# Kernel optimization log

Measured on AMD Instinct MI355X. Metric: run time of the kernel, lower is better.

Reference implementation:

```python
import jax, jax.numpy as jnp
import numpy as np

B, T, C = 4, 2048, 1024
H = 16
D = C // H  # 64


def setup_inputs() -> dict:
    key = jax.random.key(0)
    k1, k2, k3 = jax.random.split(key, 3)
    x = jax.random.normal(k1, (B, T, C), dtype=jnp.float32)
    W_attn = jax.random.normal(k2, (C, 3 * C), dtype=jnp.float32) * (1.0 / np.sqrt(C))
    W_proj = jax.random.normal(k3, (C, C), dtype=jnp.float32) * (1.0 / np.sqrt(C))
    return {"x": x, "W_attn": W_attn, "W_proj": W_proj}


def reference(x, W_attn, W_proj):
    b, t, c = x.shape
    # qkv projection: [B,T,3C]
    qkv = jnp.einsum('btc,cd->btd', x, W_attn)
    q, k, v = jnp.split(qkv, 3, axis=-1)
    # split heads -> [B,H,T,D]
    q = q.reshape(b, t, H, D).transpose(0, 2, 1, 3)
    k = k.reshape(b, t, H, D).transpose(0, 2, 1, 3)
    v = v.reshape(b, t, H, D).transpose(0, 2, 1, 3)
    # scores scaled by 1/sqrt(C) (faithful to source: uses full embed dim)
    att = jnp.einsum('bhtd,bhsd->bhts', q, k) * (1.0 / jnp.sqrt(jnp.float32(c)))
    # causal mask: -inf where key index > query index
    causal = jnp.tril(jnp.ones((t, t), dtype=bool))
    att = jnp.where(causal, att, jnp.float32(-jnp.inf))
    att = jax.nn.softmax(att, axis=-1)
    # attention output -> combine heads
    y = jnp.einsum('bhts,bhsd->bhtd', att, v)
    y = y.transpose(0, 2, 1, 3).reshape(b, t, c)
    z = jnp.einsum('btc,cd->btd', y, W_proj)
    return z
```

## Files before the change

kernel.cpp:

```cpp
#include <hip/hip_runtime.h>
#include <hip/hip_bf16.h>

typedef __bf16 bf16x8 __attribute__((ext_vector_type(8)));
typedef float f32x4 __attribute__((ext_vector_type(4)));

static __device__ __forceinline__ __bf16 tobf(float x) {
    __hip_bfloat16 h = __float2bfloat16(x);
    __bf16 r;
    __builtin_memcpy(&r, &h, 2);
    return r;
}

static __device__ __forceinline__ float fexp2(float x) {
    float r;
    asm("v_exp_f32 %0, %1" : "=v"(r) : "v"(x));
    return r;
}

__global__ __launch_bounds__(256) void prep_k(const float* __restrict__ x,
                                              __hip_bfloat16* __restrict__ x_bf,
                                              const float* __restrict__ Wa,
                                              __hip_bfloat16* __restrict__ WaT,
                                              const float* __restrict__ Wp,
                                              __hip_bfloat16* __restrict__ WpT) {
    __shared__ float tile[32][33];
    const int bid = blockIdx.x;
    const int tid = threadIdx.x;
    if (bid < 8192) {
        int i = bid * 256 + tid;
        float4 v = reinterpret_cast<const float4*>(x)[i];
        __hip_bfloat16 a = __float2bfloat16(v.x);
        __hip_bfloat16 b = __float2bfloat16(v.y);
        __hip_bfloat16 c = __float2bfloat16(v.z);
        __hip_bfloat16 d = __float2bfloat16(v.w);
        ushort4 o;
        o.x = *reinterpret_cast<unsigned short*>(&a);
        o.y = *reinterpret_cast<unsigned short*>(&b);
        o.z = *reinterpret_cast<unsigned short*>(&c);
        o.w = *reinterpret_cast<unsigned short*>(&d);
        reinterpret_cast<ushort4*>(x_bf)[i] = o;
        return;
    }
    const float* in;
    __hip_bfloat16* out;
    int bx, Cn, qrows;
    float qscale;
    int t;
    if (bid < 8192 + 3072) {
        t = bid - 8192;
        in = Wa; out = WaT; Cn = 3072; qrows = 1024;
        qscale = 0.045084223f;
        bx = t % 96;
    } else {
        t = bid - 11264;
        in = Wp; out = WpT; Cn = 1024; qrows = 0;
        qscale = 1.0f;
        bx = t % 32;
    }
    const int by = (bid < 11264) ? (t / 96) : (t / 32);
    const int R = 1024;
    const int c0 = bx * 32, r0 = by * 32;
    const int tx = tid & 31, ty = tid >> 5;
#pragma unroll
    for (int i = 0; i < 4; ++i)
        tile[ty + i * 8][tx] = in[(size_t)(r0 + ty + i * 8) * Cn + c0 + tx];
    __syncthreads();
#pragma unroll
    for (int i = 0; i < 4; ++i) {
        int orow = c0 + ty + i * 8;
        float v = tile[tx][ty + i * 8];
        if (orow < qrows) v *= qscale;
        out[(size_t)orow * R + r0 + tx] = __float2bfloat16(v);
    }
}

template <bool OUT_BF16, bool FUSE_VT>
__global__ __launch_bounds__(256, 2) void gemm4w(const __hip_bfloat16* __restrict__ A,
                                                 const __hip_bfloat16* __restrict__ Bt,
                                                 __hip_bfloat16* __restrict__ Cb,
                                                 float* __restrict__ Cf,
                                                 __hip_bfloat16* __restrict__ VtOut,
                                                 int M, int N, int K) {
    __shared__ __attribute__((aligned(16))) char As[2][128 * 128];
    __shared__ __attribute__((aligned(16))) char Bs[2][128 * 128];
    const int tid = threadIdx.x;
    const int lane = tid & 63, wid = tid >> 6;
    const int l15 = lane & 15, lg = lane >> 4;
    const int wr = wid >> 1, wc = wid & 1;
    const int lin = blockIdx.y * gridDim.x + blockIdx.x;
    const int cpx = (gridDim.x * gridDim.y) >> 3;
    const int sw = (lin & 7) * cpx + (lin >> 3);
    const int bn = sw % gridDim.x, bm = sw / gridDim.x;
    const size_t arow0 = (size_t)bm * 128;
    const size_t brow0 = (size_t)bn * 128;

    f32x4 acc[4][4] = {};

    const __hip_bfloat16* pa[4];
    const __hip_bfloat16* pb[4];
#pragma unroll
    for (int p = 0; p < 4; ++p) {
        int idx = p * 256 + tid;
        int row = idx >> 3, c = idx & 7;
        int col = 8 * (c ^ (row & 7));
        pa[p] = A + (arow0 + row) * (size_t)K + col;
        pb[p] = Bt + (brow0 + row) * (size_t)K + col;
    }

    auto stage = [&](int buf) {
        char* Ad = buf ? &As[1][0] : &As[0][0];
        char* Bd = buf ? &Bs[1][0] : &Bs[0][0];
#pragma unroll
        for (int p = 0; p < 4; ++p) {
            __builtin_amdgcn_global_load_lds(
                (const __attribute__((address_space(1))) void*)pa[p],
                (__attribute__((address_space(3))) void*)(Ad + (p * 256 + tid) * 16), 16, 0, 0);
            __builtin_amdgcn_global_load_lds(
                (const __attribute__((address_space(1))) void*)pb[p],
                (__attribute__((address_space(3))) void*)(Bd + (p * 256 + tid) * 16), 16, 0, 0);
            pa[p] += 64;
            pb[p] += 64;
        }
    };

    stage(0);
    asm volatile("s_waitcnt vmcnt(0)" ::: "memory");
    __syncthreads();

    const int nk = K >> 6;
    int cur = 0;
    for (int kt = 0; kt < nk; ++kt) {
        if (kt + 1 < nk) stage(cur ^ 1);
        const char* Ab = cur ? &As[1][0] : &As[0][0];
        const char* Bb = cur ? &Bs[1][0] : &Bs[0][0];
#pragma unroll
        for (int ks = 0; ks < 2; ++ks) {
            bf16x8 af[4], bfr[4];
#pragma unroll
            for (int mf = 0; mf < 4; ++mf) {
                int R = wr * 64 + mf * 16 + l15;
                af[mf] = *reinterpret_cast<const bf16x8*>(
                    Ab + R * 128 + 16 * ((ks * 4 + lg) ^ (R & 7)));
            }
#pragma unroll
            for (int nf = 0; nf < 4; ++nf) {
                int R = wc * 64 + nf * 16 + l15;
                bfr[nf] = *reinterpret_cast<const bf16x8*>(
                    Bb + R * 128 + 16 * ((ks * 4 + lg) ^ (R & 7)));
            }
            __builtin_amdgcn_s_setprio(1);
#pragma unroll
            for (int mf = 0; mf < 4; ++mf)
#pragma unroll
                for (int nf = 0; nf < 4; ++nf)
                    acc[mf][nf] = __builtin_amdgcn_mfma_f32_16x16x32_bf16(af[mf], bfr[nf],
                                                                          acc[mf][nf], 0, 0, 0);
            __builtin_amdgcn_s_setprio(0);
        }
        asm volatile("s_waitcnt vmcnt(0)" ::: "memory");
        __syncthreads();
        cur ^= 1;
    }

    if (FUSE_VT && bn >= 16) {
        const int trow0 = bm * 128;
        const int b = trow0 >> 11;
        const int t0 = trow0 & 2047;
        const int cv0 = bn * 128 - 2048;
        __hip_bfloat16* lds = reinterpret_cast<__hip_bfloat16*>(&As[0][0]);
#pragma unroll 1
        for (int pass = 0; pass < 2; ++pass) {
            __syncthreads();
            if (wr == pass) {
#pragma unroll
                for (int mf = 0; mf < 4; ++mf)
#pragma unroll
                    for (int nf = 0; nf < 4; ++nf)
#pragma unroll
                        for (int j = 0; j < 4; ++j) {
                            int rloc = mf * 16 + lg * 4 + j;
                            int col = wc * 64 + nf * 16 + l15;
                            lds[rloc * 136 + col] = __float2bfloat16(acc[mf][nf][j]);
                        }
            }
            __syncthreads();
#pragma unroll
            for (int q = 0; q < 4; ++q) {
                int u = q * 256 + tid;
                int vr = u >> 3, oc = u & 7;
                bf16x8 o;
#pragma unroll
                for (int e = 0; e < 8; ++e) {
                    int s = oc * 8 + e;
                    int slot = s & 31;
                    int r = (slot & 3) | (((slot >> 3) & 3) << 2) | (((slot >> 2) & 1) << 4);
                    int tsrc = (s & 32) | r;
                    o[e] = tobf(__bfloat162float(lds[tsrc * 136 + vr]));
                }
                size_t vrow = (size_t)b * 1024 + cv0 + vr;
                *reinterpret_cast<bf16x8*>(&VtOut[vrow * 2048 + t0 + pass * 64 + oc * 8]) = o;
            }
        }
        return;
    }

#pragma unroll
    for (int mf = 0; mf < 4; ++mf) {
#pragma unroll
        for (int nf = 0; nf < 4; ++nf) {
#pragma unroll
            for (int j = 0; j < 4; ++j) {
                int row = bm * 128 + wr * 64 + mf * 16 + lg * 4 + j;
                int col = bn * 128 + wc * 64 + nf * 16 + l15;
                if (OUT_BF16)
                    Cb[(size_t)row * N + col] = __float2bfloat16(acc[mf][nf][j]);
                else
                    Cf[(size_t)row * N + col] = acc[mf][nf][j];
            }
        }
    }
}

__global__ __launch_bounds__(256) void attn_k(const __hip_bfloat16* __restrict__ qkv,
                                              const __hip_bfloat16* __restrict__ Vt,
                                              __hip_bfloat16* __restrict__ y) {
    constexpr int TT = 2048;
    constexpr int S3C = 3072;
    const int bh = blockIdx.x, b = bh >> 4, h = bh & 15;
    const int st = 15 - (int)blockIdx.y;
    const int tid = threadIdx.x;
    const int wid = tid >> 6, lane = tid & 63;
    const int l15 = lane & 15, lg = lane >> 4;

    __shared__ __attribute__((aligned(16))) char Ks[2][64 * 128];
    __shared__ __attribute__((aligned(16))) char Vs[2][64 * 128];

    const __hip_bfloat16* base = qkv + (size_t)b * TT * S3C;
    const int qo = h * 64, ko = 1024 + h * 64;
    const __hip_bfloat16* vt = Vt + (size_t)bh * 64 * TT;

    bf16x8 vones;
#pragma unroll
    for (int i = 0; i < 8; ++i) vones[i] = tobf(1.0f);

    const int idx0 = tid, idx1 = 256 + tid;
    const int r0 = idx0 >> 3, c0 = 8 * ((idx0 & 7) ^ (r0 & 7));
    const int r1 = idx1 >> 3, c1 = 8 * ((idx1 & 7) ^ (r1 & 7));

    const int qbase = st * 128 + wid * 32;
    const int my_nt = (qbase >> 6) + 1;
    const int blk_nt = st * 2 + 2;

    bf16x8 aq[2][2];
#pragma unroll
    for (int m = 0; m < 2; ++m) {
        const __hip_bfloat16* qp = base + (size_t)(qbase + m * 16 + l15) * S3C + qo + lg * 8;
        aq[m][0] = *reinterpret_cast<const bf16x8*>(qp);
        aq[m][1] = *reinterpret_cast<const bf16x8*>(qp + 32);
    }

    f32x4 acc[2][4] = {};
    f32x4 lsum[2] = {};

    const __hip_bfloat16* kp0 = base + (size_t)r0 * S3C + ko + c0;
    const __hip_bfloat16* kp1 = base + (size_t)r1 * S3C + ko + c1;
    const __hip_bfloat16* vp0 = vt + (size_t)r0 * TT + c0;
    const __hip_bfloat16* vp1 = vt + (size_t)r1 * TT + c1;

    auto stage = [&](int buf) {
        char* Kd = buf ? &Ks[1][0] : &Ks[0][0];
        char* Vd = buf ? &Vs[1][0] : &Vs[0][0];
        __builtin_amdgcn_global_load_lds(
            (const __attribute__((address_space(1))) void*)kp0,
            (__attribute__((address_space(3))) void*)(Kd + idx0 * 16), 16, 0, 0);
        __builtin_amdgcn_global_load_lds(
            (const __attribute__((address_space(1))) void*)kp1,
            (__attribute__((address_space(3))) void*)(Kd + idx1 * 16), 16, 0, 0);
        __builtin_amdgcn_global_load_lds(
            (const __attribute__((address_space(1))) void*)vp0,
            (__attribute__((address_space(3))) void*)(Vd + idx0 * 16), 16, 0, 0);
        __builtin_amdgcn_global_load_lds(
            (const __attribute__((address_space(1))) void*)vp1,
            (__attribute__((address_space(3))) void*)(Vd + idx1 * 16), 16, 0, 0);
        kp0 += (size_t)64 * S3C;
        kp1 += (size_t)64 * S3C;
        vp0 += 64;
        vp1 += 64;
    };

    stage(0);
    asm volatile("s_waitcnt vmcnt(0)" ::: "memory");
    __syncthreads();

    int cur = 0;
    for (int kt = 0; kt < blk_nt; ++kt) {
        if (kt + 1 < blk_nt) stage(cur ^ 1);
        if (kt < my_nt) {
            const int kb = kt * 64;
            const char* Kb = cur ? &Ks[1][0] : &Ks[0][0];
            const char* Vb = cur ? &Vs[1][0] : &Vs[0][0];
            const int swl = l15 & 7;
            f32x4 s[2][4];
            __builtin_amdgcn_s_setprio(1);
#pragma unroll
            for (int cg = 0; cg < 4; ++cg) {
                const char* krow = Kb + (cg * 16 + l15) * 128;
                bf16x8 k0 = *reinterpret_cast<const bf16x8*>(krow + 16 * (lg ^ swl));
                bf16x8 k1 = *reinterpret_cast<const bf16x8*>(krow + 16 * ((4 + lg) ^ swl));
#pragma unroll
                for (int m = 0; m < 2; ++m) {
                    f32x4 z = {0.f, 0.f, 0.f, 0.f};
                    z = __builtin_amdgcn_mfma_f32_16x16x32_bf16(k0, aq[m][0], z, 0, 0, 0);
                    z = __builtin_amdgcn_mfma_f32_16x16x32_bf16(k1, aq[m][1], z, 0, 0, 0);
                    s[m][cg] = z;
                }
            }
            __builtin_amdgcn_s_setprio(0);
            bf16x8 vb[2][4];
#pragma unroll
            for (int dg = 0; dg < 4; ++dg) {
                const char* vrow = Vb + (dg * 16 + l15) * 128;
                vb[0][dg] = *reinterpret_cast<const bf16x8*>(vrow + 16 * (lg ^ swl));
                vb[1][dg] = *reinterpret_cast<const bf16x8*>(vrow + 16 * ((4 + lg) ^ swl));
            }
            float p[2][4][4];
            const bool needmask = (kb + 63 > qbase);
#pragma unroll
            for (int m = 0; m < 2; ++m)
#pragma unroll
                for (int cg = 0; cg < 4; ++cg)
#pragma unroll
                    for (int j = 0; j < 4; ++j) {
                        float e = fexp2(s[m][cg][j]);
                        if (needmask) {
                            int key = kb + cg * 16 + lg * 4 + j;
                            int qrow = qbase + m * 16 + l15;
                            e = (key > qrow) ? 0.f : e;
                        }
                        p[m][cg][j] = e;
                    }
            bf16x8 pa[2][2];
#pragma unroll
            for (int m = 0; m < 2; ++m)
#pragma unroll
                for (int ks = 0; ks < 2; ++ks) {
                    bf16x8 tt2;
                    tt2[0] = tobf(p[m][2 * ks][0]);
                    tt2[1] = tobf(p[m][2 * ks][1]);
                    tt2[2] = tobf(p[m][2 * ks][2]);
                    tt2[3] = tobf(p[m][2 * ks][3]);
                    tt2[4] = tobf(p[m][2 * ks + 1][0]);
                    tt2[5] = tobf(p[m][2 * ks + 1][1]);
                    tt2[6] = tobf(p[m][2 * ks + 1][2]);
                    tt2[7] = tobf(p[m][2 * ks + 1][3]);
                    pa[m][ks] = tt2;
                }
            __builtin_amdgcn_s_setprio(1);
#pragma unroll
            for (int ks = 0; ks < 2; ++ks) {
#pragma unroll
                for (int dg = 0; dg < 4; ++dg)
#pragma unroll
                    for (int m = 0; m < 2; ++m)
                        acc[m][dg] = __builtin_amdgcn_mfma_f32_16x16x32_bf16(
                            pa[m][ks], vb[ks][dg], acc[m][dg], 0, 0, 0);
#pragma unroll
                for (int m = 0; m < 2; ++m)
                    lsum[m] = __builtin_amdgcn_mfma_f32_16x16x32_bf16(pa[m][ks], vones,
                                                                      lsum[m], 0, 0, 0);
            }
            __builtin_amdgcn_s_setprio(0);
        }
        asm volatile("s_waitcnt vmcnt(0)" ::: "memory");
        __syncthreads();
        cur ^= 1;
    }

#pragma unroll
    for (int m = 0; m < 2; ++m)
#pragma unroll
        for (int j = 0; j < 4; ++j) {
            float inv = 1.f / lsum[m][j];
            int t = qbase + m * 16 + lg * 4 + j;
#pragma unroll
            for (int dg = 0; dg < 4; ++dg) {
                float o = acc[m][dg][j] * inv;
                y[((size_t)(b * TT + t)) * 1024 + h * 64 + dg * 16 + l15] = __float2bfloat16(o);
            }
        }
}

extern "C" void kernel_launch(void* const* d_in, const int* in_sizes, int n_in,
                              void* d_out, int out_size, void* d_ws, size_t ws_size,
                              hipStream_t stream) {
    const float* x = (const float*)d_in[0];
    const float* Wa = (const float*)d_in[1];
    const float* Wp = (const float*)d_in[2];
    float* out = (float*)d_out;

    __hip_bfloat16* ws = (__hip_bfloat16*)d_ws;
    __hip_bfloat16* x_bf = ws;
    __hip_bfloat16* WaT = x_bf + (size_t)8192 * 1024;
    __hip_bfloat16* WpT = WaT + (size_t)3072 * 1024;
    __hip_bfloat16* qkv = WpT + (size_t)1024 * 1024;
    __hip_bfloat16* ybf = qkv + (size_t)8192 * 3072;
    __hip_bfloat16* Vt = ybf + (size_t)8192 * 1024;

    prep_k<<<8192 + 3072 + 1024, 256, 0, stream>>>(x, x_bf, Wa, WaT, Wp, WpT);
    gemm4w<true, true><<<dim3(24, 64), 256, 0, stream>>>(x_bf, WaT, qkv, nullptr, Vt,
                                                         8192, 3072, 1024);
    attn_k<<<dim3(64, 16), 256, 0, stream>>>(qkv, Vt, ybf);
    gemm4w<false, false><<<dim3(8, 64), 256, 0, stream>>>(ybf, WpT, nullptr, out, nullptr,
                                                          8192, 1024, 1024);
}
```

Before: 160.2 us.

## Use two waves per attention block with 64 query rows each

The attention kernel now launches 128 threads (two wavefronts) per block instead of four. Each wave owns 64 query rows instead of 32, so every K/V fragment read from LDS is reused across four row groups rather than two. Per-row processing is restructured so QK^T, exp, pack and PV run per 16-row group, which keeps register pressure in check. The cost is more loads per thread when staging tiles, fewer waves to hide latency, and coarser causal-skip granularity, since each wave now covers a 64-row span.

Result: no change. 163.3 us (+1.9%).

```diff
diff --git a/kernel.cpp b/kernel.cpp
--- a/kernel.cpp
+++ b/kernel.cpp
@@ -221,9 +221,9 @@
     }
 }
 
-__global__ __launch_bounds__(256) void attn_k(const __hip_bfloat16* __restrict__ qkv,
-                                              const __hip_bfloat16* __restrict__ Vt,
-                                              __hip_bfloat16* __restrict__ y) {
+__global__ __launch_bounds__(128, 2) void attn_k(const __hip_bfloat16* __restrict__ qkv,
+                                                 const __hip_bfloat16* __restrict__ Vt,
+                                                 __hip_bfloat16* __restrict__ y) {
     constexpr int TT = 2048;
     constexpr int S3C = 3072;
     const int bh = blockIdx.x, b = bh >> 4, h = bh & 15;
@@ -243,49 +243,46 @@
 #pragma unroll
     for (int i = 0; i < 8; ++i) vones[i] = tobf(1.0f);
 
-    const int idx0 = tid, idx1 = 256 + tid;
-    const int r0 = idx0 >> 3, c0 = 8 * ((idx0 & 7) ^ (r0 & 7));
-    const int r1 = idx1 >> 3, c1 = 8 * ((idx1 & 7) ^ (r1 & 7));
-
-    const int qbase = st * 128 + wid * 32;
+    const int qbase = st * 128 + wid * 64;
     const int my_nt = (qbase >> 6) + 1;
     const int blk_nt = st * 2 + 2;
 
-    bf16x8 aq[2][2];
-#pragma unroll
-    for (int m = 0; m < 2; ++m) {
+    bf16x8 aq[4][2];
+#pragma unroll
+    for (int m = 0; m < 4; ++m) {
         const __hip_bfloat16* qp = base + (size_t)(qbase + m * 16 + l15) * S3C + qo + lg * 8;
         aq[m][0] = *reinterpret_cast<const bf16x8*>(qp);
         aq[m][1] = *reinterpret_cast<const bf16x8*>(qp + 32);
     }
 
-    f32x4 acc[2][4] = {};
-    f32x4 lsum[2] = {};
-
-    const __hip_bfloat16* kp0 = base + (size_t)r0 * S3C + ko + c0;
-    const __hip_bfloat16* kp1 = base + (size_t)r1 * S3C + ko + c1;
-    const __hip_bfloat16* vp0 = vt + (size_t)r0 * TT + c0;
-    const __hip_bfloat16* vp1 = vt + (size_t)r1 * TT + c1;
+    f32x4 acc[4][4] = {};
+    f32x4 lsum[4] = {};
+
+    const __hip_bfloat16* kp[4];
+    const __hip_bfloat16* vp[4];
+#pragma unroll
+    for (int p = 0; p < 4; ++p) {
+        int idx = p * 128 + tid;
+        int row = idx >> 3, c = idx & 7;
+        int col = 8 * (c ^ (row & 7));
+        kp[p] = base + (size_t)row * S3C + ko + col;
+        vp[p] = vt + (size_t)row * TT + col;
+    }
 
     auto stage = [&](int buf) {
         char* Kd = buf ? &Ks[1][0] : &Ks[0][0];
         char* Vd = buf ? &Vs[1][0] : &Vs[0][0];
-        __builtin_amdgcn_global_load_lds(
-            (const __attribute__((address_space(1))) void*)kp0,
-            (__attribute__((address_space(3))) void*)(Kd + idx0 * 16), 16, 0, 0);
-        __builtin_amdgcn_global_load_lds(
-            (const __attribute__((address_space(1))) void*)kp1,
-            (__attribute__((address_space(3))) void*)(Kd + idx1 * 16), 16, 0, 0);
-        __builtin_amdgcn_global_load_lds(
-            (const __attribute__((address_space(1))) void*)vp0,
-            (__attribute__((address_space(3))) void*)(Vd + idx0 * 16), 16, 0, 0);
-        __builtin_amdgcn_global_load_lds(
-            (const __attribute__((address_space(1))) void*)vp1,
-            (__attribute__((address_space(3))) void*)(Vd + idx1 * 16), 16, 0, 0);
-        kp0 += (size_t)64 * S3C;
-        kp1 += (size_t)64 * S3C;
-        vp0 += 64;
-        vp1 += 64;
+#pragma unroll
+        for (int p = 0; p < 4; ++p) {
+            __builtin_amdgcn_global_load_lds(
+                (const __attribute__((address_space(1))) void*)kp[p],
+                (__attribute__((address_space(3))) void*)(Kd + (p * 128 + tid) * 16), 16, 0, 0);
+            __builtin_amdgcn_global_load_lds(
+                (const __attribute__((address_space(1))) void*)vp[p],
+                (__attribute__((address_space(3))) void*)(Vd + (p * 128 + tid) * 16), 16, 0, 0);
+            kp[p] += (size_t)64 * S3C;
+            vp[p] += 64;
+        }
     };
 
     stage(0);
@@ -300,22 +297,13 @@
             const char* Kb = cur ? &Ks[1][0] : &Ks[0][0];
             const char* Vb = cur ? &Vs[1][0] : &Vs[0][0];
             const int swl = l15 & 7;
-            f32x4 s[2][4];
-            __builtin_amdgcn_s_setprio(1);
+            bf16x8 kf[4][2];
 #pragma unroll
             for (int cg = 0; cg < 4; ++cg) {
                 const char* krow = Kb + (cg * 16 + l15) * 128;
-                bf16x8 k0 = *reinterpret_cast<const bf16x8*>(krow + 16 * (lg ^ swl));
-                bf16x8 k1 = *reinterpret_cast<const bf16x8*>(krow + 16 * ((4 + lg) ^ swl));
-#pragma unroll
-                for (int m = 0; m < 2; ++m) {
-                    f32x4 z = {0.f, 0.f, 0.f, 0.f};
-                    z = __builtin_amdgcn_mfma_f32_16x16x32_bf16(k0, aq[m][0], z, 0, 0, 0);
-                    z = __builtin_amdgcn_mfma_f32_16x16x32_bf16(k1, aq[m][1], z, 0, 0, 0);
-                    s[m][cg] = z;
-                }
-            }
-            __builtin_amdgcn_s_setprio(0);
+                kf[cg][0] = *reinterpret_cast<const bf16x8*>(krow + 16 * (lg ^ swl));
+                kf[cg][1] = *reinterpret_cast<const bf16x8*>(krow + 16 * ((4 + lg) ^ swl));
+            }
             bf16x8 vb[2][4];
 #pragma unroll
             for (int dg = 0; dg < 4; ++dg) {
@@ -323,53 +311,58 @@
                 vb[0][dg] = *reinterpret_cast<const bf16x8*>(vrow + 16 * (lg ^ swl));
                 vb[1][dg] = *reinterpret_cast<const bf16x8*>(vrow + 16 * ((4 + lg) ^ swl));
             }
-            float p[2][4][4];
             const bool needmask = (kb + 63 > qbase);
 #pragma unroll
-            for (int m = 0; m < 2; ++m)
+            for (int m = 0; m < 4; ++m) {
+                f32x4 s[4];
+                __builtin_amdgcn_s_setprio(1);
+#pragma unroll
+                for (int cg = 0; cg < 4; ++cg) {
+                    f32x4 z = {0.f, 0.f, 0.f, 0.f};
+                    z = __builtin_amdgcn_mfma_f32_16x16x32_bf16(kf[cg][0], aq[m][0], z, 0, 0, 0);
+                    z = __builtin_amdgcn_mfma_f32_16x16x32_bf16(kf[cg][1], aq[m][1], z, 0, 0, 0);
+                    s[cg] = z;
+                }
+                __builtin_amdgcn_s_setprio(0);
+                float p[4][4];
 #pragma unroll
                 for (int cg = 0; cg < 4; ++cg)
 #pragma unroll
                     for (int j = 0; j < 4; ++j) {
-                        float e = fexp2(s[m][cg][j]);
+                        float e = fexp2(s[cg][j]);
                         if (needmask) {
                             int key = kb + cg * 16 + lg * 4 + j;
                             int qrow = qbase + m * 16 + l15;
                             e = (key > qrow) ? 0.f : e;
                         }
-                        p[m][cg][j] = e;
+                        p[cg][j] = e;
                     }
-            bf16x8 pa[2][2];
-#pragma unroll
-            for (int m = 0; m < 2; ++m)
+                bf16x8 pa[2];
 #pragma unroll
                 for (int ks = 0; ks < 2; ++ks) {
-                    bf16x8 tt2;
-                    tt2[0] = tobf(p[m][2 * ks][0]);
-                    tt2[1] = tobf(p[m][2 * ks][1]);
-                    tt2[2] = tobf(p[m][2 * ks][2]);
-                    tt2[3] = tobf(p[m][2 * ks][3]);
-                    tt2[4] = tobf(p[m][2 * ks + 1][0]);
-                    tt2[5] = tobf(p[m][2 * ks + 1][1]);
-                    tt2[6] = tobf(p[m][2 * ks + 1][2]);
-                    tt2[7] = tobf(p[m][2 * ks + 1][3]);
-                    pa[m][ks] = tt2;
+                    bf16x8 t2;
+                    t2[0] = tobf(p[2 * ks][0]);
+                    t2[1] = tobf(p[2 * ks][1]);
+                    t2[2] = tobf(p[2 * ks][2]);
+                    t2[3] = tobf(p[2 * ks][3]);
+                    t2[4] = tobf(p[2 * ks + 1][0]);
+                    t2[5] = tobf(p[2 * ks + 1][1]);
+                    t2[6] = tobf(p[2 * ks + 1][2]);
+                    t2[7] = tobf(p[2 * ks + 1][3]);
+                    pa[ks] = t2;
                 }
-            __builtin_amdgcn_s_setprio(1);
-#pragma unroll
-            for (int ks = 0; ks < 2; ++ks) {
-#pragma unroll
-                for (int dg = 0; dg < 4; ++dg)
-#pragma unroll
-                    for (int m = 0; m < 2; ++m)
+                __builtin_amdgcn_s_setprio(1);
+#pragma unroll
+                for (int ks = 0; ks < 2; ++ks) {
+#pragma unroll
+                    for (int dg = 0; dg < 4; ++dg)
                         acc[m][dg] = __builtin_amdgcn_mfma_f32_16x16x32_bf16(
-                            pa[m][ks], vb[ks][dg], acc[m][dg], 0, 0, 0);
-#pragma unroll
-                for (int m = 0; m < 2; ++m)
-                    lsum[m] = __builtin_amdgcn_mfma_f32_16x16x32_bf16(pa[m][ks], vones,
+                            pa[ks], vb[ks][dg], acc[m][dg], 0, 0, 0);
+                    lsum[m] = __builtin_amdgcn_mfma_f32_16x16x32_bf16(pa[ks], vones,
                                                                       lsum[m], 0, 0, 0);
-            }
-            __builtin_amdgcn_s_setprio(0);
+                }
+                __builtin_amdgcn_s_setprio(0);
+            }
         }
         asm volatile("s_waitcnt vmcnt(0)" ::: "memory");
         __syncthreads();
@@ -377,7 +370,7 @@
     }
 
 #pragma unroll
-    for (int m = 0; m < 2; ++m)
+    for (int m = 0; m < 4; ++m)
 #pragma unroll
         for (int j = 0; j < 4; ++j) {
             float inv = 1.f / lsum[m][j];
@@ -409,7 +402,7 @@
     prep_k<<<8192 + 3072 + 1024, 256, 0, stream>>>(x, x_bf, Wa, WaT, Wp, WpT);
     gemm4w<true, true><<<dim3(24, 64), 256, 0, stream>>>(x_bf, WaT, qkv, nullptr, Vt,
                                                          8192, 3072, 1024);
-    attn_k<<<dim3(64, 16), 256, 0, stream>>>(qkv, Vt, ybf);
+    attn_k<<<dim3(64, 16), 128, 0, stream>>>(qkv, Vt, ybf);
     gemm4w<false, false><<<dim3(8, 64), 256, 0, stream>>>(ybf, WpT, nullptr, out, nullptr,
                                                           8192, 1024, 1024);
 }
```
